# Performance work log

Hardware: AMD Instinct MI355X
Metric: run time of the kernel (lower is better)

The kernel has to match this reference:

```python
import jax, jax.numpy as jnp
import numpy as np

FEAT_STRIDE = 16
SCALES = np.array([8.0, 16.0, 32.0])
RATIOS = np.array([0.5, 1.0, 2.0])
PRE_NMS = 6000
POST_NMS = 300
NMS_THRESH = 0.7


def generate_anchors(base_size, ratios, scales):
    base = np.array([0.0, 0.0, base_size - 1.0, base_size - 1.0])

    def whctrs(a):
        w = a[2] - a[0] + 1.0
        h = a[3] - a[1] + 1.0
        return w, h, a[0] + 0.5 * (w - 1.0), a[1] + 0.5 * (h - 1.0)

    def mk(ws, hs, xc, yc):
        ws = ws[:, None]
        hs = hs[:, None]
        return np.hstack((xc - 0.5 * (ws - 1.0), yc - 0.5 * (hs - 1.0),
                          xc + 0.5 * (ws - 1.0), yc + 0.5 * (hs - 1.0)))

    w, h, xc, yc = whctrs(base)
    size = w * h
    size_ratios = size / ratios
    ws = np.round(np.sqrt(size_ratios))
    hs = np.round(ws * ratios)
    ratio_anchors = mk(ws, hs, xc, yc)
    out = []
    for a in ratio_anchors:
        w, h, xc, yc = whctrs(a)
        out.append(mk(w * scales, h * scales, xc, yc))
    return np.vstack(out).astype(np.float32)


def bbox_transform_inv(boxes, deltas):
    # boxes [..., 4], deltas [..., 4]
    w = boxes[..., 2] - boxes[..., 0] + 1.0
    h = boxes[..., 3] - boxes[..., 1] + 1.0
    cx = boxes[..., 0] + 0.5 * w
    cy = boxes[..., 1] + 0.5 * h
    pcx = deltas[..., 0] * w + cx
    pcy = deltas[..., 1] * h + cy
    pw = jnp.exp(deltas[..., 2]) * w
    ph = jnp.exp(deltas[..., 3]) * h
    return jnp.stack([pcx - 0.5 * pw, pcy - 0.5 * ph,
                      pcx + 0.5 * pw, pcy + 0.5 * ph], axis=-1)


def clip_boxes(boxes, im_info):
    # boxes [B, N, 4], im_info [B, 3] = (height, width, scale)
    hmax = (im_info[:, 0] - 1.0)[:, None]
    wmax = (im_info[:, 1] - 1.0)[:, None]
    x1 = jnp.clip(boxes[..., 0], 0.0, wmax)
    y1 = jnp.clip(boxes[..., 1], 0.0, hmax)
    x2 = jnp.clip(boxes[..., 2], 0.0, wmax)
    y2 = jnp.clip(boxes[..., 3], 0.0, hmax)
    return jnp.stack([x1, y1, x2, y2], axis=-1)


def nms_single(boxes, scores):
    # greedy NMS: boxes [M,4] already sorted desc by score, scores [M]
    M = boxes.shape[0]
    x1, y1, x2, y2 = boxes[:, 0], boxes[:, 1], boxes[:, 2], boxes[:, 3]
    areas = (x2 - x1 + 1.0) * (y2 - y1 + 1.0)
    idxs = jnp.arange(M)
    neg_inf = jnp.array(-jnp.inf, scores.dtype)

    def body(i, state):
        s, out = state
        j = jnp.argmax(s)
        valid = s[j] > neg_inf
        box = boxes[j]
        out = out.at[i].set(jnp.where(valid, box, jnp.zeros_like(box)))
        xx1 = jnp.maximum(box[0], x1)
        yy1 = jnp.maximum(box[1], y1)
        xx2 = jnp.minimum(box[2], x2)
        yy2 = jnp.minimum(box[3], y2)
        inter = jnp.maximum(0.0, xx2 - xx1 + 1.0) * jnp.maximum(0.0, yy2 - yy1 + 1.0)
        iou = inter / (areas[j] + areas - inter)
        sup = (iou > NMS_THRESH) | (idxs == j)
        s = jnp.where(valid & sup, neg_inf, s)
        return (s, out)

    out0 = jnp.zeros((POST_NMS, 4), boxes.dtype)
    _, out = jax.lax.fori_loop(0, POST_NMS, body, (scores, out0))
    return out


def setup_inputs() -> dict:
    key = jax.random.key(0)
    k1, k2 = jax.random.split(key)
    B, A, H, W = 16, 9, 100, 150
    scores = jax.random.normal(k1, (B, 2 * A, H, W), dtype=jnp.float32)
    bbox_deltas = 0.25 * jax.random.normal(k2, (B, 4 * A, H, W), dtype=jnp.float32)
    im_info = jnp.tile(jnp.array([[1600.0, 2400.0, 1.0]], dtype=jnp.float32), (B, 1))
    return {"scores": scores, "bbox_deltas": bbox_deltas, "im_info": im_info}


def reference(scores, bbox_deltas, im_info):
    B, C, H, W = scores.shape
    anchors_base = jnp.asarray(generate_anchors(FEAT_STRIDE, RATIOS, SCALES))
    A = anchors_base.shape[0]
    scores_fg = scores[:, A:, :, :]                       # [B, A, H, W]
    # anchor shifts over the feature grid
    sx, sy = jnp.meshgrid(jnp.arange(W) * FEAT_STRIDE, jnp.arange(H) * FEAT_STRIDE)
    shifts = jnp.stack([sx.ravel(), sy.ravel(), sx.ravel(), sy.ravel()], axis=1).astype(scores.dtype)  # [K,4]
    anchors = (anchors_base[None, :, :] + shifts[:, None, :]).reshape(-1, 4)  # [K*A, 4]
    deltas = bbox_deltas.transpose(0, 2, 3, 1).reshape(B, -1, 4)             # [B, K*A, 4]
    scr = scores_fg.transpose(0, 2, 3, 1).reshape(B, -1)                     # [B, K*A]
    proposals = bbox_transform_inv(anchors[None, :, :], deltas)
    proposals = clip_boxes(proposals, im_info)
    # sort desc, keep top pre_nms
    top_scores, order = jax.lax.top_k(scr, PRE_NMS)
    props_top = jnp.take_along_axis(proposals, order[..., None], axis=1)     # [B, PRE_NMS, 4]
    kept = jax.vmap(nms_single)(props_top, top_scores)                       # [B, POST_NMS, 4]
    batch_idx = jnp.broadcast_to(
        jnp.arange(B, dtype=scores.dtype)[:, None, None], (B, POST_NMS, 1))
    return jnp.concatenate([batch_idx, kept], axis=2)                        # [B, POST_NMS, 5]
```

## Files before the change

### kernel.cpp

```cpp
#include <hip/hip_runtime.h>
#include <cstdint>
#include <cmath>

#define HWSZ    15000
#define W_FEAT  150
#define A_NUM   9
#define NPER    135000
#define B_NUM   16
#define PRE_NMS 6000
#define POST_NMS 300
#define NBINS   16384
#define GCAP    2048

__device__ __constant__ float ANC[9][4] = {
    {-84.f,  -40.f,  99.f,  55.f},
    {-176.f, -88.f, 191.f, 103.f},
    {-360.f,-184.f, 375.f, 199.f},
    {-56.f,  -56.f,  71.f,  71.f},
    {-120.f,-120.f, 135.f, 135.f},
    {-248.f,-248.f, 263.f, 263.f},
    {-36.f,  -80.f,  51.f,  95.f},
    {-80.f, -168.f,  95.f, 183.f},
    {-168.f,-344.f, 183.f, 359.f}};

__device__ __forceinline__ uint32_t fkey(float s) {
    uint32_t u = __float_as_uint(s);
    return (u & 0x80000000u) ? ~u : (u | 0x80000000u);
}

__device__ __forceinline__ bool iou_gt(const float4& q, float qa,
                                       const float4& c, float ca) {
    float xx1 = fmaxf(q.x, c.x);
    float yy1 = fmaxf(q.y, c.y);
    float xx2 = fminf(q.z, c.z);
    float yy2 = fminf(q.w, c.w);
    float iw = fmaxf(0.0f, __fadd_rn(__fsub_rn(xx2, xx1), 1.0f));
    float ih = fmaxf(0.0f, __fadd_rn(__fsub_rn(yy2, yy1), 1.0f));
    float inter = __fmul_rn(iw, ih);
    float den = __fsub_rn(__fadd_rn(qa, ca), inter);
    return (double)inter >= 0x1.666667p-1 * (double)den;
}

__device__ __forceinline__ float area_of(const float4& c) {
    return __fmul_rn(__fadd_rn(__fsub_rn(c.z, c.x), 1.0f),
                     __fadd_rn(__fsub_rn(c.w, c.y), 1.0f));
}

__global__ __launch_bounds__(1024) void k_hist(const float* __restrict__ scores,
                                               uint32_t* __restrict__ subhist) {
    __shared__ uint32_t hist[NBINS];
    int b = blockIdx.y, sx = blockIdx.x, S = gridDim.x, tid = threadIdx.x;
    for (int i = tid; i < NBINS; i += 1024) hist[i] = 0;
    __syncthreads();
    const float4* sc4 = (const float4*)(scores + (size_t)(b * 18 + 9) * HWSZ);
    int nf4 = NPER / 4;
    int per = (nf4 + S - 1) / S;
    int lo = sx * per, hi = min(lo + per, nf4);
    for (int i = lo + tid; i < hi; i += 1024) {
        float4 v = sc4[i];
        atomicAdd(&hist[fkey(v.x) >> 18], 1u);
        atomicAdd(&hist[fkey(v.y) >> 18], 1u);
        atomicAdd(&hist[fkey(v.z) >> 18], 1u);
        atomicAdd(&hist[fkey(v.w) >> 18], 1u);
    }
    __syncthreads();
    uint32_t* out = subhist + ((size_t)b * S + sx) * NBINS;
    for (int i = tid; i < NBINS; i += 1024) out[i] = hist[i];
}

__global__ __launch_bounds__(1024) void k_scan(const uint32_t* __restrict__ subhist,
                                               int S, uint32_t* __restrict__ scum,
                                               uint32_t* __restrict__ gbase) {
    __shared__ uint32_t tl[NBINS];
    __shared__ uint32_t psum[1024];
    __shared__ uint32_t gb[8];
    int b = blockIdx.x, tid = threadIdx.x;
    for (int i = tid; i < NBINS; i += 1024) {
        uint32_t t = 0;
        for (int u = 0; u < S; ++u) t += subhist[((size_t)b * S + u) * NBINS + i];
        tl[i] = t;
    }
    if (tid < 8) gb[tid] = 0xFFFFFFFFu;
    __syncthreads();
    int base = NBINS - 16 * (tid + 1);
    uint32_t csum = 0;
#pragma unroll
    for (int i = 0; i < 16; ++i) csum += tl[base + i];
    psum[tid] = csum;
    __syncthreads();
    for (int off = 1; off < 1024; off <<= 1) {
        uint32_t v = (tid >= off) ? psum[tid - off] : 0u;
        __syncthreads();
        psum[tid] += v;
        __syncthreads();
    }
    uint32_t c = tid ? psum[tid - 1] : 0u;
    for (int i = 15; i >= 0; --i) {
        uint32_t t = tl[base + i];
        scum[(size_t)b * NBINS + base + i] = c;
        if (t && c < PRE_NMS) atomicMin(&gb[c >> 10], c);
        c += t;
    }
    __syncthreads();
    if (tid < 8) gbase[b * 8 + tid] = gb[tid];
}

__global__ __launch_bounds__(1024) void k_group(
        const float* __restrict__ scores, const float* __restrict__ deltas,
        const float* __restrict__ im_info, const uint32_t* __restrict__ scum,
        const uint32_t* __restrict__ gbase, float4* __restrict__ boxes) {
    __shared__ uint32_t sl[NBINS];
    __shared__ uint64_t s[GCAP];
    __shared__ uint32_t lcnt;
    int b = blockIdx.y, g = blockIdx.x, tid = threadIdx.x;
    uint32_t base = gbase[b * 8 + g];
    if (base == 0xFFFFFFFFu) return;
    for (int i = tid; i < NBINS; i += 1024) sl[i] = scum[(size_t)b * NBINS + i];
    for (int i = tid; i < GCAP; i += 1024) s[i] = ~0ull;
    if (tid == 0) lcnt = 0;
    __syncthreads();
    uint32_t glo = (uint32_t)g << 10;
    uint32_t ghi = min(glo + 1024u, (uint32_t)PRE_NMS);
    const float4* sc4 = (const float4*)(scores + (size_t)(b * 18 + 9) * HWSZ);
    for (int i = tid; i < NPER / 4; i += 1024) {
        float4 v = sc4[i];
        float cc[4] = {v.x, v.y, v.z, v.w};
#pragma unroll
        for (int c = 0; c < 4; ++c) {
            uint32_t k = fkey(cc[c]);
            uint32_t sc = sl[k >> 18];
            if (sc >= glo && sc < ghi) {
                uint32_t pos = atomicAdd(&lcnt, 1u);
                if (pos < GCAP) {
                    int e = 4 * i + c;
                    int a = e / HWSZ, p = e - a * HWSZ;
                    s[pos] = ((uint64_t)(~k) << 32) | (uint32_t)(p * A_NUM + a);
                }
            }
        }
    }
    __syncthreads();
    int cnt = (int)min(lcnt, (uint32_t)GCAP);
    for (unsigned k = 2; k <= GCAP; k <<= 1) {
        for (unsigned j = k >> 1; j; j >>= 1) {
            unsigned p = tid;
            unsigned i = ((p & ~(j - 1)) << 1) | (p & (j - 1));
            unsigned ixj = i | j;
            uint64_t x = s[i], y = s[ixj];
            bool up = ((i & k) == 0);
            if (up ? (x > y) : (x < y)) { s[i] = y; s[ixj] = x; }
            __syncthreads();
        }
    }
    float him = im_info[b * 3 + 0], wim = im_info[b * 3 + 1];
    float ymax = __fsub_rn(him, 1.0f), xmax = __fsub_rn(wim, 1.0f);
    for (int r = tid; r < GCAP; r += 1024) {
        uint32_t P = base + (uint32_t)r;
        uint32_t idx = (uint32_t)s[r];
        if (r < cnt && P < PRE_NMS && idx < NPER) {
            int a = idx % A_NUM;
            int p = idx / A_NUM;
            int wc = p % W_FEAT, hr = p / W_FEAT;
            float ax1 = ANC[a][0] + (float)(wc * 16);
            float ay1 = ANC[a][1] + (float)(hr * 16);
            float ax2 = ANC[a][2] + (float)(wc * 16);
            float ay2 = ANC[a][3] + (float)(hr * 16);
            const float* dp = deltas + (size_t)(b * 36 + a * 4) * HWSZ + p;
            float dx = dp[0], dy = dp[HWSZ], dw = dp[2 * HWSZ], dh = dp[3 * HWSZ];
            float ww = __fadd_rn(__fsub_rn(ax2, ax1), 1.0f);
            float hh = __fadd_rn(__fsub_rn(ay2, ay1), 1.0f);
            float cx = __fadd_rn(ax1, __fmul_rn(0.5f, ww));
            float cy = __fadd_rn(ay1, __fmul_rn(0.5f, hh));
            float pcx = __fadd_rn(__fmul_rn(dx, ww), cx);
            float pcy = __fadd_rn(__fmul_rn(dy, hh), cy);
            float ew = (float)exp((double)dw);
            float eh = (float)exp((double)dh);
            float pw = __fmul_rn(ew, ww);
            float ph = __fmul_rn(eh, hh);
            float x1 = __fsub_rn(pcx, __fmul_rn(0.5f, pw));
            float y1 = __fsub_rn(pcy, __fmul_rn(0.5f, ph));
            float x2 = __fadd_rn(pcx, __fmul_rn(0.5f, pw));
            float y2 = __fadd_rn(pcy, __fmul_rn(0.5f, ph));
            float4 bx;
            bx.x = fminf(fmaxf(x1, 0.0f), xmax);
            bx.y = fminf(fmaxf(y1, 0.0f), ymax);
            bx.z = fminf(fmaxf(x2, 0.0f), xmax);
            bx.w = fminf(fmaxf(y2, 0.0f), ymax);
            boxes[(size_t)b * PRE_NMS + P] = bx;
        }
    }
}

__global__ __launch_bounds__(256) void k_mask(const float4* __restrict__ boxes,
                                              uint64_t* __restrict__ masks,
                                              int NC, int NW, int T) {
    int b = blockIdx.y;
    int wv = threadIdx.x >> 6, lane = threadIdx.x & 63;
    int t = blockIdx.x * 4 + wv;
    if (t >= T) return;
    int ti = 0, rem = t;
    while (rem >= NW - ti) { rem -= NW - ti; ++ti; }
    int tj = ti + rem;
    __shared__ float4 colb[4][64];
    __shared__ float  cola[4][64];
    const float4* bb = boxes + (size_t)b * PRE_NMS;
    int i = ti * 64 + lane;
    float4 c = bb[i];
    float ca = area_of(c);
    float4 q0 = bb[tj * 64 + lane];
    colb[wv][lane] = q0;
    cola[wv][lane] = area_of(q0);
    asm volatile("s_waitcnt lgkmcnt(0)" ::: "memory");
    __builtin_amdgcn_wave_barrier();
    uint64_t m = 0;
    if (ti == tj) {
#pragma unroll
        for (int jj = 0; jj < 64; ++jj) {
            bool hit = (jj > lane) && iou_gt(colb[wv][jj], cola[wv][jj], c, ca);
            m |= ((uint64_t)(hit ? 1u : 0u)) << jj;
        }
    } else {
#pragma unroll
        for (int jj = 0; jj < 64; ++jj) {
            bool hit = iou_gt(colb[wv][jj], cola[wv][jj], c, ca);
            m |= ((uint64_t)(hit ? 1u : 0u)) << jj;
        }
    }
    masks[((size_t)b * NW + tj) * NC + i] = m;
}

#define PROC(P)                                                                \
    do {                                                                       \
        float ca = area_of(P);                                                 \
        bool viol = false;                                                     \
        if (K > 0)   viol |= (lane       < K) & iou_gt(k0, a0, P, ca);         \
        if (K > 64)  viol |= (lane + 64  < K) & iou_gt(k1, a1, P, ca);         \
        if (K > 128) viol |= (lane + 128 < K) & iou_gt(k2, a2, P, ca);         \
        if (K > 192) viol |= (lane + 192 < K) & iou_gt(k3, a3, P, ca);         \
        if (K > 256) viol |= (lane + 256 < K) & iou_gt(k4, a4, P, ca);         \
        if (!__any((int)viol)) {                                               \
            int sl = K >> 6, tg = K & 63;                                      \
            if (lane == tg) {                                                  \
                switch (sl) {                                                  \
                case 0: k0 = P; a0 = ca; break;                                \
                case 1: k1 = P; a1 = ca; break;                                \
                case 2: k2 = P; a2 = ca; break;                                \
                case 3: k3 = P; a3 = ca; break;                                \
                default: k4 = P; a4 = ca; break;                               \
                }                                                              \
            }                                                                  \
            ++K;                                                               \
        }                                                                      \
    } while (0)

#define RSTEP(RG)                                                              \
    do {                                                                       \
        if (!fin && i < NC) {                                                  \
            bool mine = (lane == (i >> 6));                                    \
            bool sb = mine && ((sup >> (i & 63)) & 1ull);                      \
            if (!__any((int)sb)) {                                             \
                int sl = K >> 6, tg = K & 63;                                  \
                if (lane == tg) {                                              \
                    switch (sl) {                                              \
                    case 0: i0 = i; break;                                     \
                    case 1: i1 = i; break;                                     \
                    case 2: i2 = i; break;                                     \
                    case 3: i3 = i; break;                                     \
                    default: i4 = i; break;                                    \
                    }                                                          \
                }                                                              \
                if (lane < NW) sup |= RG;                                      \
                ++K;                                                           \
                if (K >= POST_NMS) fin = true;                                 \
            }                                                                  \
            int nx = i + 8; if (nx >= NC) nx = NC - 1;                         \
            RG = mrow[nx];                                                     \
            ++i;                                                               \
        }                                                                      \
    } while (0)

__global__ __launch_bounds__(64) void k_resolve(const float4* __restrict__ boxes,
                                                const uint64_t* __restrict__ masks,
                                                int NC, int NW,
                                                float* __restrict__ out) {
    int b = blockIdx.x, lane = threadIdx.x;
    const float4* bb = boxes + (size_t)b * PRE_NMS;
    int K = 0;
    int i0 = 0, i1 = 0, i2 = 0, i3 = 0, i4 = 0;
    bool fin = false;

    if (NC > 0) {
        const uint64_t* mrow =
            masks + ((size_t)b * NW + (lane < NW ? lane : NW - 1)) * NC;
        uint64_t sup = 0;
        uint64_t r0 = mrow[0], r1 = mrow[1], r2 = mrow[2], r3 = mrow[3];
        uint64_t r4 = mrow[4], r5 = mrow[5], r6 = mrow[6], r7 = mrow[7];
        int i = 0;
        while (i < NC && !fin) {
            RSTEP(r0); RSTEP(r1); RSTEP(r2); RSTEP(r3);
            RSTEP(r4); RSTEP(r5); RSTEP(r6); RSTEP(r7);
        }
    }

    float4 k0, k1, k2, k3, k4;
    float a0, a1, a2, a3, a4;
    { int id = (lane       < K) ? i0 : 0; k0 = bb[id]; a0 = area_of(k0); }
    { int id = (lane + 64  < K) ? i1 : 0; k1 = bb[id]; a1 = area_of(k1); }
    { int id = (lane + 128 < K) ? i2 : 0; k2 = bb[id]; a2 = area_of(k2); }
    { int id = (lane + 192 < K) ? i3 : 0; k3 = bb[id]; a3 = area_of(k3); }
    { int id = (lane + 256 < K) ? i4 : 0; k4 = bb[id]; a4 = area_of(k4); }

    if (!fin && NC < PRE_NMS) {
        float4 p0 = bb[NC + 0], p1 = bb[NC + 1], p2 = bb[NC + 2], p3 = bb[NC + 3];
        bool done = false;
        for (int r = NC; r < PRE_NMS && !done; r += 4) {
            int n = r + 4;
            float4 n0 = bb[(n + 0 < PRE_NMS) ? n + 0 : PRE_NMS - 1];
            float4 n1 = bb[(n + 1 < PRE_NMS) ? n + 1 : PRE_NMS - 1];
            float4 n2 = bb[(n + 2 < PRE_NMS) ? n + 2 : PRE_NMS - 1];
            float4 n3 = bb[(n + 3 < PRE_NMS) ? n + 3 : PRE_NMS - 1];
            PROC(p0); if (K >= POST_NMS) done = true;
            if (!done) { PROC(p1); if (K >= POST_NMS) done = true; }
            if (!done) { PROC(p2); if (K >= POST_NMS) done = true; }
            if (!done) { PROC(p3); if (K >= POST_NMS) done = true; }
            p0 = n0; p1 = n1; p2 = n2; p3 = n3;
        }
    }

#pragma unroll
    for (int s = 0; s < 5; ++s) {
        int idx = s * 64 + lane;
        if (idx < POST_NMS) {
            float4 c;
            switch (s) {
            case 0: c = k0; break;
            case 1: c = k1; break;
            case 2: c = k2; break;
            case 3: c = k3; break;
            default: c = k4; break;
            }
            bool v = idx < K;
            float* o = out + (size_t)(b * POST_NMS + idx) * 5;
            o[0] = (float)b;
            o[1] = v ? c.x : 0.f;
            o[2] = v ? c.y : 0.f;
            o[3] = v ? c.z : 0.f;
            o[4] = v ? c.w : 0.f;
        }
    }
}

extern "C" void kernel_launch(void* const* d_in, const int* in_sizes, int n_in,
                              void* d_out, int out_size, void* d_ws, size_t ws_size,
                              hipStream_t stream) {
    const float* scores  = (const float*)d_in[0];
    const float* deltas  = (const float*)d_in[1];
    const float* im_info = (const float*)d_in[2];
    float* out = (float*)d_out;
    char* ws = (char*)d_ws;

    const size_t boxB  = (size_t)B_NUM * PRE_NMS * 16;
    const size_t scumB = (size_t)B_NUM * NBINS * 4;
    const size_t fixedB = boxB + scumB + 4096;
    int NC = 0, S = 1;
    const int lad[2] = {2048, 1024};
    for (int li = 0; li < 2 && !NC; ++li) {
        size_t mb = 2ull * lad[li] * lad[li];
        if (fixedB + 1048576ull + mb <= ws_size) {
            NC = lad[li];
            for (int ss = 8; ss >= 1; ss >>= 1)
                if (fixedB + (size_t)ss * 1048576ull + mb <= ws_size) { S = ss; break; }
        }
    }
    if (!NC) { NC = 1024; S = 1; }
    int NW = NC / 64;

    float4*   boxes   = (float4*)ws;
    uint32_t* scum    = (uint32_t*)(ws + boxB);
    uint32_t* gbase   = (uint32_t*)(ws + boxB + scumB);
    uint32_t* subhist = (uint32_t*)(ws + fixedB);
    uint64_t* masks   = (uint64_t*)(ws + fixedB + (size_t)S * 1048576ull);

    dim3 gh(S, B_NUM);
    k_hist<<<gh, 1024, 0, stream>>>(scores, subhist);
    k_scan<<<B_NUM, 1024, 0, stream>>>(subhist, S, scum, gbase);
    dim3 gg(6, B_NUM);
    k_group<<<gg, 1024, 0, stream>>>(scores, deltas, im_info, scum, gbase, boxes);
    int T = NW * (NW + 1) / 2;
    dim3 gm((T + 3) / 4, B_NUM);
    k_mask<<<gm, 256, 0, stream>>>(boxes, masks, NC, NW, T);
    k_resolve<<<B_NUM, 64, 0, stream>>>(boxes, masks, NC, NW, out);
}
```

Before: 170.7 us.

## Add compaction kernel so group sort reads candidates instead of rescanning scores

```diff
diff --git a/kernel.cpp b/kernel.cpp
--- a/kernel.cpp
+++ b/kernel.cpp
@@ -11,6 +11,7 @@
 #define POST_NMS 300
 #define NBINS   16384
 #define GCAP    2048
+#define NGRP    6
 
 __device__ __constant__ float ANC[9][4] = {
     {-84.f,  -40.f,  99.f,  55.f},
@@ -105,42 +106,72 @@
     if (tid < 8) gbase[b * 8 + tid] = gb[tid];
 }
 
+__global__ __launch_bounds__(1024) void k_compact(
+        const float* __restrict__ scores, const uint32_t* __restrict__ scum,
+        uint64_t* __restrict__ cand, uint32_t* __restrict__ gcnt) {
+    __shared__ uint32_t sl[NBINS];
+    __shared__ uint32_t lc[NGRP], lb[NGRP];
+    int b = blockIdx.y, sx = blockIdx.x, S = gridDim.x, tid = threadIdx.x;
+    for (int i = tid; i < NBINS; i += 1024) sl[i] = scum[(size_t)b * NBINS + i];
+    if (tid < NGRP) lc[tid] = 0;
+    __syncthreads();
+    const float4* sc4 = (const float4*)(scores + (size_t)(b * 18 + 9) * HWSZ);
+    int nf4 = NPER / 4;
+    int per = (nf4 + S - 1) / S;
+    int lo = sx * per, hi = min(lo + per, nf4);
+    for (int i0 = lo; i0 < hi; i0 += 1024) {
+        int i = i0 + tid;
+        bool w[4];
+        uint32_t gg[4], pp[4];
+        uint64_t rec[4];
+#pragma unroll
+        for (int c = 0; c < 4; ++c) w[c] = false;
+        if (i < hi) {
+            float4 v = sc4[i];
+            float cc[4] = {v.x, v.y, v.z, v.w};
+#pragma unroll
+            for (int c = 0; c < 4; ++c) {
+                uint32_t k = fkey(cc[c]);
+                uint32_t sc = sl[k >> 18];
+                if (sc < PRE_NMS) {
+                    w[c] = true;
+                    gg[c] = sc >> 10;
+                    pp[c] = atomicAdd(&lc[gg[c]], 1u);
+                    int e = 4 * i + c;
+                    int a = e / HWSZ, p = e - a * HWSZ;
+                    rec[c] = ((uint64_t)(~k) << 32) | (uint32_t)(p * A_NUM + a);
+                }
+            }
+        }
+        __syncthreads();
+        if (tid < NGRP && lc[tid])
+            lb[tid] = atomicAdd(&gcnt[(b * NGRP + tid) * 16], lc[tid]);
+        __syncthreads();
+#pragma unroll
+        for (int c = 0; c < 4; ++c)
+            if (w[c]) {
+                uint32_t pos = lb[gg[c]] + pp[c];
+                if (pos < GCAP)
+                    cand[((size_t)b * NGRP + gg[c]) * GCAP + pos] = rec[c];
+            }
+        __syncthreads();
+        if (tid < NGRP) lc[tid] = 0;
+        __syncthreads();
+    }
+}
+
 __global__ __launch_bounds__(1024) void k_group(
-        const float* __restrict__ scores, const float* __restrict__ deltas,
-        const float* __restrict__ im_info, const uint32_t* __restrict__ scum,
+        const uint64_t* __restrict__ cand, const uint32_t* __restrict__ gcnt,
+        const float* __restrict__ deltas, const float* __restrict__ im_info,
         const uint32_t* __restrict__ gbase, float4* __restrict__ boxes) {
-    __shared__ uint32_t sl[NBINS];
     __shared__ uint64_t s[GCAP];
-    __shared__ uint32_t lcnt;
     int b = blockIdx.y, g = blockIdx.x, tid = threadIdx.x;
     uint32_t base = gbase[b * 8 + g];
     if (base == 0xFFFFFFFFu) return;
-    for (int i = tid; i < NBINS; i += 1024) sl[i] = scum[(size_t)b * NBINS + i];
-    for (int i = tid; i < GCAP; i += 1024) s[i] = ~0ull;
-    if (tid == 0) lcnt = 0;
-    __syncthreads();
-    uint32_t glo = (uint32_t)g << 10;
-    uint32_t ghi = min(glo + 1024u, (uint32_t)PRE_NMS);
-    const float4* sc4 = (const float4*)(scores + (size_t)(b * 18 + 9) * HWSZ);
-    for (int i = tid; i < NPER / 4; i += 1024) {
-        float4 v = sc4[i];
-        float cc[4] = {v.x, v.y, v.z, v.w};
-#pragma unroll
-        for (int c = 0; c < 4; ++c) {
-            uint32_t k = fkey(cc[c]);
-            uint32_t sc = sl[k >> 18];
-            if (sc >= glo && sc < ghi) {
-                uint32_t pos = atomicAdd(&lcnt, 1u);
-                if (pos < GCAP) {
-                    int e = 4 * i + c;
-                    int a = e / HWSZ, p = e - a * HWSZ;
-                    s[pos] = ((uint64_t)(~k) << 32) | (uint32_t)(p * A_NUM + a);
-                }
-            }
-        }
-    }
-    __syncthreads();
-    int cnt = (int)min(lcnt, (uint32_t)GCAP);
+    uint32_t cnt = min(gcnt[(b * NGRP + g) * 16], (uint32_t)GCAP);
+    for (int i = tid; i < GCAP; i += 1024)
+        s[i] = (i < (int)cnt) ? cand[((size_t)b * NGRP + g) * GCAP + i] : ~0ull;
+    __syncthreads();
     for (unsigned k = 2; k <= GCAP; k <<= 1) {
         for (unsigned j = k >> 1; j; j >>= 1) {
             unsigned p = tid;
@@ -157,7 +188,7 @@
     for (int r = tid; r < GCAP; r += 1024) {
         uint32_t P = base + (uint32_t)r;
         uint32_t idx = (uint32_t)s[r];
-        if (r < cnt && P < PRE_NMS && idx < NPER) {
+        if (r < (int)cnt && P < PRE_NMS && idx < NPER) {
             int a = idx % A_NUM;
             int p = idx / A_NUM;
             int wc = p % W_FEAT, hr = p / W_FEAT;
@@ -359,17 +390,19 @@
     float* out = (float*)d_out;
     char* ws = (char*)d_ws;
 
-    const size_t boxB  = (size_t)B_NUM * PRE_NMS * 16;
-    const size_t scumB = (size_t)B_NUM * NBINS * 4;
-    const size_t fixedB = boxB + scumB + 4096;
+    const size_t boxB   = (size_t)B_NUM * PRE_NMS * 16;
+    const size_t scumB  = (size_t)B_NUM * NBINS * 4;
+    const size_t metaB  = 8192;
+    const size_t candB  = (size_t)B_NUM * NGRP * GCAP * 8;
+    const size_t fixedB = boxB + scumB + metaB;
     int NC = 0, S = 1;
     const int lad[2] = {2048, 1024};
     for (int li = 0; li < 2 && !NC; ++li) {
         size_t mb = 2ull * lad[li] * lad[li];
-        if (fixedB + 1048576ull + mb <= ws_size) {
+        if (fixedB + 1048576ull + candB + mb <= ws_size) {
             NC = lad[li];
             for (int ss = 8; ss >= 1; ss >>= 1)
-                if (fixedB + (size_t)ss * 1048576ull + mb <= ws_size) { S = ss; break; }
+                if (fixedB + (size_t)ss * 1048576ull + candB + mb <= ws_size) { S = ss; break; }
         }
     }
     if (!NC) { NC = 1024; S = 1; }
@@ -378,14 +411,19 @@
     float4*   boxes   = (float4*)ws;
     uint32_t* scum    = (uint32_t*)(ws + boxB);
     uint32_t* gbase   = (uint32_t*)(ws + boxB + scumB);
+    uint32_t* gcnt    = (uint32_t*)(ws + boxB + scumB + 1024);
     uint32_t* subhist = (uint32_t*)(ws + fixedB);
-    uint64_t* masks   = (uint64_t*)(ws + fixedB + (size_t)S * 1048576ull);
+    uint64_t* cand    = (uint64_t*)(ws + fixedB + (size_t)S * 1048576ull);
+    uint64_t* masks   = (uint64_t*)(ws + fixedB + (size_t)S * 1048576ull + candB);
+
+    hipMemsetAsync(gcnt, 0, (size_t)B_NUM * NGRP * 16 * 4, stream);
 
     dim3 gh(S, B_NUM);
     k_hist<<<gh, 1024, 0, stream>>>(scores, subhist);
     k_scan<<<B_NUM, 1024, 0, stream>>>(subhist, S, scum, gbase);
-    dim3 gg(6, B_NUM);
-    k_group<<<gg, 1024, 0, stream>>>(scores, deltas, im_info, scum, gbase, boxes);
+    k_compact<<<gh, 1024, 0, stream>>>(scores, scum, cand, gcnt);
+    dim3 gg(NGRP, B_NUM);
+    k_group<<<gg, 1024, 0, stream>>>(cand, gcnt, deltas, im_info, gbase, boxes);
     int T = NW * (NW + 1) / 2;
     dim3 gm((T + 3) / 4, B_NUM);
     k_mask<<<gm, 256, 0, stream>>>(boxes, masks, NC, NW, T);
```

New measurement: 162.0 us. 5.1% less time.
